# Kernel optimization log

Hardware: AMD Instinct MI355X
Metric: run time of the kernel (lower is better)

Reference implementation:

```python
import jax, jax.numpy as jnp
import numpy as np

B = 16384
D = 1024          # in_features
R = 64            # low_rank
E = 4             # num_experts
L = 3             # layer_num


def setup_inputs() -> dict:
    key = jax.random.key(0)
    ks = jax.random.split(key, 6)
    # xavier-normal-ish scales
    s_uv = (2.0 / (D + R)) ** 0.5
    s_c = (2.0 / (R + R)) ** 0.5
    s_g = (2.0 / (D + 1)) ** 0.5
    return {
        "inputs": jax.random.normal(ks[0], (B, D), dtype=jnp.float32),
        "U": jax.random.normal(ks[1], (L, E, D, R), dtype=jnp.float32) * s_uv,
        "V": jax.random.normal(ks[2], (L, E, D, R), dtype=jnp.float32) * s_uv,
        "C": jax.random.normal(ks[3], (L, E, R, R), dtype=jnp.float32) * s_c,
        "gate_w": jax.random.normal(ks[4], (E, D), dtype=jnp.float32) * s_g,
        "bias": jnp.zeros((L, D), dtype=jnp.float32),
    }


def reference(inputs, U, V, C, gate_w, bias):
    x0 = inputs                                  # [B, D]
    x_l = x0
    for i in range(L):
        # gating: per-expert Linear(d,1) on x_l -> [B, E], softmax over experts
        gates = jax.nn.softmax(x_l @ gate_w.T, axis=1)        # [B, E]
        # v_x = tanh(V_e^T x_l) for all experts at once
        v = jnp.tanh(jnp.einsum('bd,edr->ber', x_l, V[i]))    # [B, E, R]
        v = jnp.tanh(jnp.einsum('ers,bes->ber', C[i], v))     # [B, E, R]
        uv = jnp.einsum('edr,ber->bed', U[i], v)              # [B, E, D]
        dot = x0[:, None, :] * (uv + bias[i][None, None, :])  # [B, E, D]
        moe_out = jnp.einsum('bed,be->bd', dot, gates)        # [B, D]
        x_l = moe_out + x_l
    return x_l
```

## Files before the change

kernel.cpp:

```cpp
#include <hip/hip_runtime.h>
#include <math.h>

#define BB 16384
#define DD 1024
#define RR 64
#define EE 4
#define ER 256
#define LL 3

#define LDM 72

typedef __bf16 bf16x8 __attribute__((ext_vector_type(8)));
typedef float f32x4 __attribute__((ext_vector_type(4)));
typedef unsigned short us;

static __device__ inline us f2b(float f) {
    union { float f; unsigned u; } c; c.f = f;
    return (us)((c.u + 0x7FFF + ((c.u >> 16) & 1)) >> 16);
}
static __device__ inline float b2f(us v) {
    union { unsigned u; float f; } c; c.u = ((unsigned)v) << 16;
    return c.f;
}
static __device__ inline float fast_tanh(float x) {
    float t = __expf(2.f * x);
    return 1.f - 2.f / (t + 1.f);
}
static __device__ __forceinline__ void ld_lds16(const us* g, us* l) {
    __builtin_amdgcn_global_load_lds((const __attribute__((address_space(1))) void*)g,
                                     (__attribute__((address_space(3))) void*)l, 16, 0, 0);
}

__global__ __launch_bounds__(256) void convF2B(const float* __restrict__ s, us* __restrict__ d) {
    int f = (blockIdx.x * 256 + threadIdx.x) * 4;
    float4 v = *(const float4*)&s[f];
    *(ushort4*)&d[f] = make_ushort4(f2b(v.x), f2b(v.y), f2b(v.z), f2b(v.w));
}
__global__ __launch_bounds__(256) void convV(const float* __restrict__ V, us* __restrict__ Vt) {
    const int le = blockIdx.x;
    const int d0 = blockIdx.y * 64;
    __shared__ float t[64 * 65];
    const int tid = threadIdx.x;
    const float* Vb = V + (size_t)le * DD * RR;
    #pragma unroll
    for (int p = 0; p < 4; ++p) {
        int f = tid + p * 256; int dd = f >> 4; int c = (f & 15) * 4;
        float4 v = *(const float4*)&Vb[(size_t)(d0 + dd) * RR + c];
        t[dd * 65 + c + 0] = v.x; t[dd * 65 + c + 1] = v.y;
        t[dd * 65 + c + 2] = v.z; t[dd * 65 + c + 3] = v.w;
    }
    __syncthreads();
    int r = tid >> 2, dg = (tid & 3) * 16;
    us o[16];
    #pragma unroll
    for (int k = 0; k < 16; ++k) o[k] = f2b(t[(dg + k) * 65 + r]);
    us* dst = Vt + (size_t)le * RR * DD + (size_t)r * DD + d0 + dg;
    #pragma unroll
    for (int q = 0; q < 4; ++q) *(ushort4*)&dst[q * 4] = *(ushort4*)&o[q * 4];
}

__global__ __launch_bounds__(512, 2) void layer_fused(const us* __restrict__ xs,
                                                      const us* __restrict__ Vt,
                                                      const us* __restrict__ Ce,
                                                      const us* __restrict__ gwb,
                                                      const us* __restrict__ x0b,
                                                      const us* __restrict__ Ub,
                                                      us* __restrict__ xbo,
                                                      const float* __restrict__ biasl,
                                                      float* __restrict__ out, int last) {
    const int row0 = blockIdx.x * 64;
    const int tid = threadIdx.x;
    const int lane = tid & 63, wave = tid >> 6;
    const int l15 = lane & 15, quad = lane >> 4;
    const int e = wave & 3, h = wave >> 2;
    const int e64 = e * 64;

    __shared__ __align__(16) union {
        struct { us buf[3][20480]; us gw[4096]; float gates[256]; } s;
        us Tt[4][64 * LDM];
        struct { us wlds[64 * 256]; float smf[8][1024]; } p2;
    } u;

    const bool gw4 = (wave < 4);
    const int r8   = lane >> 3;
    const int cA8  = (lane & 7) ^ r8;
    const int l7   = l15 & 7;

    ld_lds16(gwb + (size_t)(lane & 3) * DD + (wave * 16 + (lane >> 2)) * 8, &u.s.gw[wave * 512]);

    auto STAGE = [&](int bi, int k0) {
        us* bb = u.s.buf[bi];
        #pragma unroll
        for (int j = 0; j < 4; ++j) {
            int row = wave * 32 + j * 8 + r8;
            ld_lds16(Vt + (size_t)row * DD + k0 + cA8 * 8, &bb[(wave * 256 + j * 64) * 8]);
        }
        {
            int row = wave * 8 + r8;
            ld_lds16(xs + (size_t)(row0 + row) * DD + k0 + cA8 * 8, &bb[16384 + wave * 512]);
        }
    };

    f32x4 acc[4][2] = {};
    f32x4 accg = {};
    STAGE(0, 0); STAGE(1, 64);

    int cur = 0;
    for (int t = 0; t < 16; ++t) {
        if (t < 15) asm volatile("s_waitcnt vmcnt(5)" ::: "memory");
        else        asm volatile("s_waitcnt vmcnt(0)" ::: "memory");
        __builtin_amdgcn_s_barrier();
        if (t < 14) {
            int st = cur + 2; if (st >= 3) st -= 3;
            STAGE(st, (t + 2) * 64);
        }
        __builtin_amdgcn_sched_barrier(0);
        const us* bb = u.s.buf[cur];
        #pragma unroll
        for (int ks = 0; ks < 2; ++ks) {
            const int sl = ((ks * 4 + quad) ^ l7) * 8;
            bf16x8 af[4], bfr[2];
            #pragma unroll
            for (int mt = 0; mt < 4; ++mt)
                af[mt] = *(const bf16x8*)&bb[(e64 + mt * 16 + l15) * 64 + sl];
            #pragma unroll
            for (int nt = 0; nt < 2; ++nt)
                bfr[nt] = *(const bf16x8*)&bb[16384 + (h * 32 + nt * 16 + l15) * 64 + sl];
            #pragma unroll
            for (int mt = 0; mt < 4; ++mt)
                #pragma unroll
                for (int nt = 0; nt < 2; ++nt)
                    acc[mt][nt] = __builtin_amdgcn_mfma_f32_16x16x32_bf16(af[mt], bfr[nt], acc[mt][nt], 0, 0, 0);
            if (gw4) {
                bf16x8 bfrg = *(const bf16x8*)&bb[16384 + (wave * 16 + l15) * 64 + sl];
                bf16x8 afg  = *(const bf16x8*)&u.s.gw[((t * 8 + ks * 4 + quad) * 4 + (l15 & 3)) * 8];
                accg = __builtin_amdgcn_mfma_f32_16x16x32_bf16(afg, bfrg, accg, 0, 0, 0);
            }
        }
        cur = (cur == 2) ? 0 : cur + 1;
    }
    __builtin_amdgcn_s_barrier();
    __builtin_amdgcn_sched_barrier(0);

    #pragma unroll
    for (int mt = 0; mt < 4; ++mt)
        #pragma unroll
        for (int nt = 0; nt < 2; ++nt) {
            int b = h * 32 + nt * 16 + l15;
            us o[4];
            #pragma unroll
            for (int i = 0; i < 4; ++i) o[i] = f2b(fast_tanh(acc[mt][nt][i]));
            *(ushort4*)&u.Tt[e][b * LDM + mt * 16 + quad * 4] = *(ushort4*)o;
        }
    if (gw4 && quad == 0) {
        float l0 = accg[0], l1 = accg[1], l2 = accg[2], l3 = accg[3];
        float m = fmaxf(fmaxf(l0, l1), fmaxf(l2, l3));
        float g0 = __expf(l0 - m), g1 = __expf(l1 - m);
        float g2 = __expf(l2 - m), g3 = __expf(l3 - m);
        float inv = 1.f / (g0 + g1 + g2 + g3);
        int b = wave * 16 + l15;
        u.s.gates[0 * 64 + b] = g0 * inv; u.s.gates[1 * 64 + b] = g1 * inv;
        u.s.gates[2 * 64 + b] = g2 * inv; u.s.gates[3 * 64 + b] = g3 * inv;
    }
    __syncthreads();

    const us* Cb = Ce + (size_t)e * RR * RR;
    f32x4 acc2[4][2] = {};
    #pragma unroll
    for (int ks = 0; ks < 2; ++ks) {
        bf16x8 af2[4], bf2[2];
        #pragma unroll
        for (int mt = 0; mt < 4; ++mt)
            af2[mt] = *(const bf16x8*)&Cb[(size_t)(mt * 16 + l15) * RR + ks * 32 + quad * 8];
        #pragma unroll
        for (int nt = 0; nt < 2; ++nt)
            bf2[nt] = *(const bf16x8*)&u.Tt[e][(h * 32 + nt * 16 + l15) * LDM + ks * 32 + quad * 8];
        #pragma unroll
        for (int mt = 0; mt < 4; ++mt)
            #pragma unroll
            for (int nt = 0; nt < 2; ++nt)
                acc2[mt][nt] = __builtin_amdgcn_mfma_f32_16x16x32_bf16(af2[mt], bf2[nt], acc2[mt][nt], 0, 0, 0);
    }
    __syncthreads();

    #pragma unroll
    for (int mt = 0; mt < 4; ++mt)
        #pragma unroll
        for (int nt = 0; nt < 2; ++nt) {
            int b = h * 32 + nt * 16 + l15;
            float g = u.s.gates[e64 + b];
            us o[4];
            #pragma unroll
            for (int i = 0; i < 4; ++i) o[i] = f2b(g * fast_tanh(acc2[mt][nt][i]));
            int col = e64 + mt * 16 + quad * 4;
            int cc = col >> 3, off = col & 7;
            *(ushort4*)&u.p2.wlds[b * 256 + ((cc ^ (b & 7)) << 3) + off] = *(ushort4*)o;
        }
    __syncthreads();

    const int bl = lane >> 2, dc3 = lane & 3;
    #pragma unroll 1
    for (int p = 0; p < 2; ++p) {
        const int dw = p * 512 + wave * 64;
        f32x4 pac[4][4] = {};
        bf16x8 a0[4], a1[4];
        #define LOADU(dst, S) { const int e2 = (S) >> 1, r0q = ((S) & 1) * 32;            \
            _Pragma("unroll")                                                              \
            for (int mt = 0; mt < 4; ++mt) {                                               \
                int d = dw + mt * 16 + l15;                                                \
                dst[mt] = *(const bf16x8*)&Ub[((size_t)e2 * DD + d) * RR + r0q + quad * 8];\
            } }
        #define LOADW(dst, S) { const int e2 = (S) >> 1, r0q = ((S) & 1) * 32;            \
            _Pragma("unroll")                                                              \
            for (int nt = 0; nt < 4; ++nt) {                                               \
                int b = nt * 16 + l15;                                                     \
                int cc = e2 * 8 + (r0q >> 3) + quad;                                       \
                dst[nt] = *(const bf16x8*)&u.p2.wlds[b * 256 + ((cc ^ (b & 7)) << 3)];     \
            } }
        #define MM(A, W) { _Pragma("unroll")                                               \
            for (int mt = 0; mt < 4; ++mt) { _Pragma("unroll")                             \
                for (int nt = 0; nt < 4; ++nt)                                             \
                    pac[mt][nt] = __builtin_amdgcn_mfma_f32_16x16x32_bf16(A[mt], W[nt], pac[mt][nt], 0, 0, 0); } }
        LOADU(a0, 0);
        #pragma unroll
        for (int sp = 0; sp < 4; ++sp) {
            bf16x8 w0[4], w1[4];
            LOADU(a1, 2 * sp + 1);
            LOADW(w0, 2 * sp);
            MM(a0, w0);
            if (sp < 3) LOADU(a0, 2 * sp + 2);
            LOADW(w1, 2 * sp + 1);
            MM(a1, w1);
        }
        #undef LOADU
        #undef LOADW
        #undef MM

        const int dg = dw + dc3 * 16;
        uint4 X[4][2], L[4][2];
        #pragma unroll
        for (int nt = 0; nt < 4; ++nt) {
            const size_t gb = (size_t)(row0 + nt * 16 + bl) * DD + dg;
            X[nt][0] = *(const uint4*)&x0b[gb];     X[nt][1] = *(const uint4*)&x0b[gb + 8];
            L[nt][0] = *(const uint4*)&xs[gb];      L[nt][1] = *(const uint4*)&xs[gb + 8];
        }
        float bfv[16];
        *(float4*)&bfv[0]  = *(const float4*)&biasl[dg];
        *(float4*)&bfv[4]  = *(const float4*)&biasl[dg + 4];
        *(float4*)&bfv[8]  = *(const float4*)&biasl[dg + 8];
        *(float4*)&bfv[12] = *(const float4*)&biasl[dg + 12];
        float* sw = u.p2.smf[wave];
        #pragma unroll
        for (int nt = 0; nt < 4; ++nt) {
            #pragma unroll
            for (int mt = 0; mt < 4; ++mt) {
                int ch = (mt * 4 + quad) ^ (l15 & 7);
                *(f32x4*)&sw[l15 * 64 + ch * 4] = pac[mt][nt];
            }
            asm volatile("s_waitcnt lgkmcnt(0)" ::: "memory");
            __builtin_amdgcn_sched_barrier(0);
            const size_t gb = (size_t)(row0 + nt * 16 + bl) * DD + dg;
            uint xu[8], lu[8];
            *(uint4*)&xu[0] = X[nt][0]; *(uint4*)&xu[4] = X[nt][1];
            *(uint4*)&lu[0] = L[nt][0]; *(uint4*)&lu[4] = L[nt][1];
            float o[16];
            #pragma unroll
            for (int j = 0; j < 4; ++j) {
                int ch = (dc3 * 4 + j) ^ (bl & 7);
                float4 a = *(const float4*)&sw[bl * 64 + ch * 4];
                #pragma unroll
                for (int i = 0; i < 4; ++i) {
                    int k = j * 4 + i;
                    float av = (i == 0) ? a.x : (i == 1) ? a.y : (i == 2) ? a.z : a.w;
                    uint uu = xu[k >> 1], ll = lu[k >> 1];
                    float xv = b2f((k & 1) ? (us)(uu >> 16) : (us)(uu & 0xffff));
                    float xl = b2f((k & 1) ? (us)(ll >> 16) : (us)(ll & 0xffff));
                    o[k] = xv * (av + bfv[k]) + xl;
                }
            }
            if (last) {
                *(float4*)&out[gb]      = *(float4*)&o[0];
                *(float4*)&out[gb + 4]  = *(float4*)&o[4];
                *(float4*)&out[gb + 8]  = *(float4*)&o[8];
                *(float4*)&out[gb + 12] = *(float4*)&o[12];
            } else {
                us ob[16];
                #pragma unroll
                for (int k = 0; k < 16; ++k) ob[k] = f2b(o[k]);
                *(uint4*)&xbo[gb]     = *(uint4*)&ob[0];
                *(uint4*)&xbo[gb + 8] = *(uint4*)&ob[8];
            }
        }
    }
}

extern "C" void kernel_launch(void* const* d_in, const int* in_sizes, int n_in,
                              void* d_out, int out_size, void* d_ws, size_t ws_size,
                              hipStream_t stream) {
    const float* inputs = (const float*)d_in[0];
    const float* U      = (const float*)d_in[1];
    const float* V      = (const float*)d_in[2];
    const float* C      = (const float*)d_in[3];
    const float* gw     = (const float*)d_in[4];
    const float* bias   = (const float*)d_in[5];
    float* out = (float*)d_out;

    us* xb0 = (us*)d_ws;
    us* xb  = xb0 + (size_t)BB * DD;
    us* gwb = xb + (size_t)BB * DD;
    us* Vt  = gwb + (size_t)EE * DD;
    us* Ub  = Vt + (size_t)LL * EE * RR * DD;
    us* Cb  = Ub + (size_t)LL * EE * DD * RR;

    convF2B<<<dim3(BB * DD / 1024), 256, 0, stream>>>(inputs, xb0);
    convF2B<<<dim3(LL * EE * DD * RR / 1024), 256, 0, stream>>>(U, Ub);
    convF2B<<<dim3(LL * EE * RR * RR / 1024), 256, 0, stream>>>(C, Cb);
    convF2B<<<dim3(EE * DD / 1024), 256, 0, stream>>>(gw, gwb);
    convV<<<dim3(LL * EE, DD / 64), 256, 0, stream>>>(V, Vt);

    for (int i = 0; i < LL; ++i) {
        const us* xs = (i == 0) ? xb0 : xb;
        layer_fused<<<dim3(BB / 64), 512, 0, stream>>>(
            xs, Vt + (size_t)i * EE * RR * DD, Cb + (size_t)i * EE * RR * RR, gwb,
            xb0, Ub + (size_t)i * EE * DD * RR, xb, bias + (size_t)i * DD,
            out, i == LL - 1);
    }
}
```

Before: 276.5 us.

## Pre-pack U, V and C weights into MFMA fragment order for contiguous loads

The weight-conversion kernels now write U, C and V in bf16 laid out in the exact per-lane fragment order the MFMA loops consume. V is stored pre-swizzled per 64-column k-tile so each wave's LDS staging reads contiguous 512-element chunks. U and C are arranged so each lane's 16-byte fragment load is fully coalesced across the wave, where before each lane did a strided row gather. The aim is fewer memory transactions and simpler address math in the fused layer kernel. In exchange the preprocessing kernels get more complex index arithmetic, and the packed layouts must match the consumer exactly.

Result: faster. 262.3 us (-5.1%).

```diff
diff --git a/kernel.cpp b/kernel.cpp
--- a/kernel.cpp
+++ b/kernel.cpp
@@ -36,6 +36,7 @@
     float4 v = *(const float4*)&s[f];
     *(ushort4*)&d[f] = make_ushort4(f2b(v.x), f2b(v.y), f2b(v.z), f2b(v.w));
 }
+
 __global__ __launch_bounds__(256) void convV(const float* __restrict__ V, us* __restrict__ Vt) {
     const int le = blockIdx.x;
     const int d0 = blockIdx.y * 64;
@@ -54,17 +55,57 @@
     us o[16];
     #pragma unroll
     for (int k = 0; k < 16; ++k) o[k] = f2b(t[(dg + k) * 65 + r]);
-    us* dst = Vt + (size_t)le * RR * DD + (size_t)r * DD + d0 + dg;
-    #pragma unroll
-    for (int q = 0; q < 4; ++q) *(ushort4*)&dst[q * 4] = *(ushort4*)&o[q * 4];
+    const int l = le >> 2, eV = le & 3;
+    const int row = eV * 64 + r, kt = blockIdx.y;
+    us* dstL = Vt + (size_t)l * (EE * RR * DD);
+    #pragma unroll
+    for (int q = 0; q < 4; ++q) {
+        int dd = dg + q * 4;
+        int slot = ((dd >> 3) ^ row) & 7;
+        *(ushort4*)&dstL[(((size_t)kt * 256 + row) * 8 + slot) * 8 + (dd & 7)] = *(ushort4*)&o[q * 4];
+    }
+}
+
+__global__ __launch_bounds__(256) void convU(const float* __restrict__ U, us* __restrict__ Up) {
+    int gid = blockIdx.x * 256 + threadIdx.x;
+    int rb = (gid & 7) * 8;
+    int d  = (gid >> 3) & 1023;
+    int e  = (gid >> 13) & 3;
+    int l  = gid >> 15;
+    const float* s = U + (((size_t)(l * 4 + e) * 1024 + d) * 64 + rb);
+    float4 v0 = *(const float4*)&s[0], v1 = *(const float4*)&s[4];
+    us o[8] = { f2b(v0.x), f2b(v0.y), f2b(v0.z), f2b(v0.w),
+                f2b(v1.x), f2b(v1.y), f2b(v1.z), f2b(v1.w) };
+    int rh = rb >> 5, quad = (rb & 31) >> 3;
+    int lane = quad * 16 + (d & 15), dblk = d >> 4;
+    us* dst = Up + (size_t)l * (EE * DD * RR) + (size_t)(((e * 2 + rh) * 64 + dblk) * 64 + lane) * 8;
+    *(ushort4*)&dst[0] = *(ushort4*)&o[0];
+    *(ushort4*)&dst[4] = *(ushort4*)&o[4];
+}
+
+__global__ __launch_bounds__(256) void convC(const float* __restrict__ C, us* __restrict__ Cp) {
+    int gid = blockIdx.x * 256 + threadIdx.x;
+    int sb = (gid & 7) * 8;
+    int r  = (gid >> 3) & 63;
+    int e  = (gid >> 9) & 3;
+    int l  = gid >> 11;
+    const float* s = C + (((size_t)(l * 4 + e) * 64 + r) * 64 + sb);
+    float4 v0 = *(const float4*)&s[0], v1 = *(const float4*)&s[4];
+    us o[8] = { f2b(v0.x), f2b(v0.y), f2b(v0.z), f2b(v0.w),
+                f2b(v1.x), f2b(v1.y), f2b(v1.z), f2b(v1.w) };
+    int ks = sb >> 5, quad = (sb & 31) >> 3;
+    int lane = quad * 16 + (r & 15), mt = r >> 4;
+    us* dst = Cp + (size_t)l * (EE * RR * RR) + (size_t)(((e * 2 + ks) * 4 + mt) * 64 + lane) * 8;
+    *(ushort4*)&dst[0] = *(ushort4*)&o[0];
+    *(ushort4*)&dst[4] = *(ushort4*)&o[4];
 }
 
 __global__ __launch_bounds__(512, 2) void layer_fused(const us* __restrict__ xs,
-                                                      const us* __restrict__ Vt,
-                                                      const us* __restrict__ Ce,
+                                                      const us* __restrict__ Vp,
+                                                      const us* __restrict__ Cp,
                                                       const us* __restrict__ gwb,
                                                       const us* __restrict__ x0b,
-                                                      const us* __restrict__ Ub,
+                                                      const us* __restrict__ Up,
                                                       us* __restrict__ xbo,
                                                       const float* __restrict__ biasl,
                                                       float* __restrict__ out, int last) {
@@ -90,11 +131,10 @@
 
     auto STAGE = [&](int bi, int k0) {
         us* bb = u.s.buf[bi];
-        #pragma unroll
-        for (int j = 0; j < 4; ++j) {
-            int row = wave * 32 + j * 8 + r8;
-            ld_lds16(Vt + (size_t)row * DD + k0 + cA8 * 8, &bb[(wave * 256 + j * 64) * 8]);
-        }
+        const us* vsrc = Vp + (((size_t)(k0 >> 6) * 256 + wave * 32) * 8) * 8 + lane * 8;
+        #pragma unroll
+        for (int j = 0; j < 4; ++j)
+            ld_lds16(vsrc + j * 512, &bb[(wave * 256 + j * 64) * 8]);
         {
             int row = wave * 8 + r8;
             ld_lds16(xs + (size_t)(row0 + row) * DD + k0 + cA8 * 8, &bb[16384 + wave * 512]);
@@ -164,14 +204,13 @@
     }
     __syncthreads();
 
-    const us* Cb = Ce + (size_t)e * RR * RR;
     f32x4 acc2[4][2] = {};
     #pragma unroll
     for (int ks = 0; ks < 2; ++ks) {
         bf16x8 af2[4], bf2[2];
         #pragma unroll
         for (int mt = 0; mt < 4; ++mt)
-            af2[mt] = *(const bf16x8*)&Cb[(size_t)(mt * 16 + l15) * RR + ks * 32 + quad * 8];
+            af2[mt] = *(const bf16x8*)&Cp[(size_t)(((e * 2 + ks) * 4 + mt) * 64 + lane) * 8];
         #pragma unroll
         for (int nt = 0; nt < 2; ++nt)
             bf2[nt] = *(const bf16x8*)&u.Tt[e][(h * 32 + nt * 16 + l15) * LDM + ks * 32 + quad * 8];
@@ -204,12 +243,10 @@
         const int dw = p * 512 + wave * 64;
         f32x4 pac[4][4] = {};
         bf16x8 a0[4], a1[4];
-        #define LOADU(dst, S) { const int e2 = (S) >> 1, r0q = ((S) & 1) * 32;            \
+        #define LOADU(dst, S) { const int base = (S) * 64 + p * 32 + wave * 4;             \
             _Pragma("unroll")                                                              \
-            for (int mt = 0; mt < 4; ++mt) {                                               \
-                int d = dw + mt * 16 + l15;                                                \
-                dst[mt] = *(const bf16x8*)&Ub[((size_t)e2 * DD + d) * RR + r0q + quad * 8];\
-            } }
+            for (int mt = 0; mt < 4; ++mt)                                                 \
+                dst[mt] = *(const bf16x8*)&Up[(size_t)((base + mt) * 64 + lane) * 8]; }
         #define LOADW(dst, S) { const int e2 = (S) >> 1, r0q = ((S) & 1) * 32;            \
             _Pragma("unroll")                                                              \
             for (int nt = 0; nt < 4; ++nt) {                                               \
@@ -308,21 +345,21 @@
     us* xb0 = (us*)d_ws;
     us* xb  = xb0 + (size_t)BB * DD;
     us* gwb = xb + (size_t)BB * DD;
-    us* Vt  = gwb + (size_t)EE * DD;
-    us* Ub  = Vt + (size_t)LL * EE * RR * DD;
-    us* Cb  = Ub + (size_t)LL * EE * DD * RR;
+    us* Vp  = gwb + (size_t)EE * DD;
+    us* Up  = Vp + (size_t)LL * EE * RR * DD;
+    us* Cp  = Up + (size_t)LL * EE * DD * RR;
 
     convF2B<<<dim3(BB * DD / 1024), 256, 0, stream>>>(inputs, xb0);
-    convF2B<<<dim3(LL * EE * DD * RR / 1024), 256, 0, stream>>>(U, Ub);
-    convF2B<<<dim3(LL * EE * RR * RR / 1024), 256, 0, stream>>>(C, Cb);
+    convU<<<dim3(LL * EE * DD * RR / 8 / 256), 256, 0, stream>>>(U, Up);
+    convC<<<dim3(LL * EE * RR * RR / 8 / 256), 256, 0, stream>>>(C, Cp);
     convF2B<<<dim3(EE * DD / 1024), 256, 0, stream>>>(gw, gwb);
-    convV<<<dim3(LL * EE, DD / 64), 256, 0, stream>>>(V, Vt);
+    convV<<<dim3(LL * EE, DD / 64), 256, 0, stream>>>(V, Vp);
 
     for (int i = 0; i < LL; ++i) {
         const us* xs = (i == 0) ? xb0 : xb;
         layer_fused<<<dim3(BB / 64), 512, 0, stream>>>(
-            xs, Vt + (size_t)i * EE * RR * DD, Cb + (size_t)i * EE * RR * RR, gwb,
-            xb0, Ub + (size_t)i * EE * DD * RR, xb, bias + (size_t)i * DD,
+            xs, Vp + (size_t)i * EE * RR * DD, Cp + (size_t)i * EE * RR * RR, gwb,
+            xb0, Up + (size_t)i * EE * DD * RR, xb, bias + (size_t)i * DD,
             out, i == LL - 1);
     }
 }
```
